# Optimization experiments

Measured on AMD Instinct MI355X. Metric: run time of the kernel, lower is better.

## Reference

```python
import jax, jax.numpy as jnp
import numpy as np

N_NODES = 10000
N_EDGES = 160000
DIM = 1024


def setup_inputs() -> dict:
    key = jax.random.key(0)
    k1, k2, k3 = jax.random.split(key, 3)
    x = jax.random.normal(k1, (N_NODES, DIM), dtype=jnp.float32)
    edge_index = jax.random.randint(k2, (2, N_EDGES), 0, N_NODES, dtype=jnp.int64)
    # Glorot-style init for the GCNConv weight; zero bias (PyG default)
    W = jax.random.normal(k3, (DIM, DIM), dtype=jnp.float32) * (1.0 / np.sqrt(DIM))
    b = jnp.zeros((DIM,), dtype=jnp.float32)
    return {"x": x, "edge_index": edge_index, "W": W, "b": b}


def reference(x, edge_index, W, b):
    """GCNConv (add_self_loops=True, symmetric norm) -> Dropout(eval=identity) -> ReLU."""
    n = x.shape[0]
    loops = jnp.arange(n, dtype=edge_index.dtype)
    src = jnp.concatenate([edge_index[0], loops])  # [E+N]
    dst = jnp.concatenate([edge_index[1], loops])  # [E+N]

    # symmetric normalization: deg^{-1/2}[src] * deg^{-1/2}[dst], deg on dst side
    deg = jax.ops.segment_sum(jnp.ones_like(dst, dtype=x.dtype), dst, num_segments=n)
    dinv = jnp.where(deg > 0, jax.lax.rsqrt(deg), jnp.zeros_like(deg))
    norm = dinv[src] * dinv[dst]  # [E+N]

    h = x @ W                                   # [N, D] dense transform first
    msg = h[src] * norm[:, None]                # gather + edge scaling [E+N, D]
    out = jax.ops.segment_sum(msg, dst, num_segments=n) + b  # scatter-add + bias

    # Dropout(0.5) is identity in eval mode; activation is ReLU
    return jax.nn.relu(out)
```

## Files before the change

kernel.cpp:

```cpp
#include <hip/hip_runtime.h>
#include <hip/hip_bf16.h>
#include <cstdint>
#include <cstddef>

typedef __bf16 bf16x8 __attribute__((ext_vector_type(8)));
typedef float  f32x4  __attribute__((ext_vector_type(4)));
typedef float  f32x2  __attribute__((ext_vector_type(2)));

#define D_DIM 1024
#define BM 128
#define BN 128
#define NXCD 8
#define CAP 64

#define GLB(p) ((const __attribute__((address_space(1))) void*)(p))
#define LDS(p) ((__attribute__((address_space(3))) void*)(p))

__global__ __launch_bounds__(256) void prep_kernel(
    const float* __restrict__ x, __bf16* __restrict__ xb,
    const float* __restrict__ W, __bf16* __restrict__ wT,
    const int* __restrict__ ei, int* __restrict__ cnt, int* __restrict__ col,
    int N, int MP, int E, int nconv, int ntr)
{
    int blk = blockIdx.x, tid = threadIdx.x;
    if (blk < nconv) {
        int i = blk * 256 + tid;
        int total = MP * (D_DIM / 8);
        if (i >= total) return;
        int row = i >> 7;
        size_t base = (size_t)i * 8;
        bf16x8 o;
        if (row < N) {
            float4 v0 = *(const float4*)(x + base);
            float4 v1 = *(const float4*)(x + base + 4);
            o[0] = (__bf16)v0.x; o[1] = (__bf16)v0.y; o[2] = (__bf16)v0.z; o[3] = (__bf16)v0.w;
            o[4] = (__bf16)v1.x; o[5] = (__bf16)v1.y; o[6] = (__bf16)v1.z; o[7] = (__bf16)v1.w;
        } else {
            #pragma unroll
            for (int j = 0; j < 8; ++j) o[j] = (__bf16)0.f;
        }
        *(bf16x8*)(xb + base) = o;
    } else if (blk < nconv + ntr) {
        __shared__ float tile[32][33];
        int bb = blk - nconv;
        int nb = (bb & 31) * 32, kb = (bb >> 5) * 32;
        int tx = tid & 31, ty = tid >> 5;
        #pragma unroll
        for (int i = 0; i < 32; i += 8)
            tile[ty + i][tx] = W[(size_t)(kb + ty + i) * D_DIM + nb + tx];
        __syncthreads();
        #pragma unroll
        for (int i = 0; i < 32; i += 8)
            wT[(size_t)(nb + ty + i) * D_DIM + kb + tx] = (__bf16)tile[tx][ty + i];
    } else {
        int e = (blk - nconv - ntr) * 256 + tid;
        if (e < E) {
            const int* src = ei;
            const int* dst = ei + E;
            int d = dst[e];
            int pos = atomicAdd(&cnt[d], 1);
            if (pos < CAP) col[(d << 6) + pos] = src[e] << 11;
        }
    }
}

__global__ __launch_bounds__(256) void gemmpad_kernel(
    const __bf16* __restrict__ A,
    const __bf16* __restrict__ BT,
    __bf16* __restrict__ C,
    const int* __restrict__ cnt, int* __restrict__ col, int Nn,
    int mtiles, int ntiles, int chunk, int npad)
{
    int tid = threadIdx.x;
    if ((int)blockIdx.x < npad) {
        int d = blockIdx.x * 256 + tid;
        if (d < Nn) {
            int c  = min(cnt[d], CAP);
            int p1 = (c + 7) & ~7;
            int zoff = Nn << 11;
            for (int p = c; p < p1; ++p) col[(d << 6) + p] = zoff;
        }
        return;
    }
    __shared__ __bf16 As[2][BM * 32];
    __shared__ __bf16 Bs[2][BN * 32];

    int wg = blockIdx.x - npad;
    int c8 = wg & (NXCD - 1);
    int r  = wg >> 3;
    int bm = c8 * chunk + r / ntiles;
    int bn = r % ntiles;
    if (bm >= mtiles) return;

    int wid = tid >> 6, lane = tid & 63;
    int wr = wid >> 1, wc = wid & 1;

    auto stage = [&](int h, int sel) {
        #pragma unroll
        for (int i = 0; i < 2; ++i) {
            int c   = i * 256 + tid;
            int row = c >> 2;
            int js  = (c & 3) ^ (row & 3);
            const __bf16* ga = A  + (size_t)(bm * BM + row) * D_DIM + h * 32 + js * 8;
            const __bf16* gb = BT + (size_t)(bn * BN + row) * D_DIM + h * 32 + js * 8;
            __builtin_amdgcn_global_load_lds(GLB(ga), LDS(&As[sel][c * 8]), 16, 0, 0);
            __builtin_amdgcn_global_load_lds(GLB(gb), LDS(&Bs[sel][c * 8]), 16, 0, 0);
        }
    };

    f32x4 acc[4][4] = {};
    stage(0, 0);
    asm volatile("s_waitcnt vmcnt(0)" ::: "memory");
    __syncthreads();

    const int halves = D_DIM / 32;
    for (int h = 0; h < halves; ++h) {
        int cur = h & 1;
        if (h + 1 < halves) stage(h + 1, cur ^ 1);
        bf16x8 af[4], bfr[4];
        int j = lane >> 4;
        #pragma unroll
        for (int mi = 0; mi < 4; ++mi) {
            int rr = wr * 64 + mi * 16 + (lane & 15);
            af[mi] = *(const bf16x8*)(&As[cur][rr * 32 + ((j ^ (rr & 3)) << 3)]);
        }
        #pragma unroll
        for (int ni = 0; ni < 4; ++ni) {
            int rr = wc * 64 + ni * 16 + (lane & 15);
            bfr[ni] = *(const bf16x8*)(&Bs[cur][rr * 32 + ((j ^ (rr & 3)) << 3)]);
        }
        #pragma unroll
        for (int mi = 0; mi < 4; ++mi)
            #pragma unroll
            for (int ni = 0; ni < 4; ++ni)
                acc[mi][ni] = __builtin_amdgcn_mfma_f32_16x16x32_bf16(
                    af[mi], bfr[ni], acc[mi][ni], 0, 0, 0);
        __syncthreads();
    }

    #pragma unroll
    for (int mi = 0; mi < 4; ++mi)
        #pragma unroll
        for (int rr = 0; rr < 4; ++rr) {
            int row = bm * BM + wr * 64 + mi * 16 + (lane >> 4) * 4 + rr;
            float dvr = 0.0f;
            if (row < Nn) dvr = rsqrtf((float)min(cnt[row], CAP) + 1.0f);
            #pragma unroll
            for (int ni = 0; ni < 4; ++ni) {
                int colc = bn * BN + wc * 64 + ni * 16 + (lane & 15);
                C[(size_t)row * D_DIM + colc] = (__bf16)(acc[mi][ni][rr] * dvr);
            }
        }
}

__global__ __launch_bounds__(256) void scatter_kernel(
    const __bf16* __restrict__ h, const int* __restrict__ cnt,
    const int* __restrict__ col, const float* __restrict__ bias,
    float* __restrict__ out, int N)
{
    int blk = blockIdx.x;
    int c   = blk & (NXCD - 1);
    int q   = blk >> 3;
    int wid = threadIdx.x >> 6, lane = threadIdx.x & 63;
    int d = q * 4 + wid;
    if (d >= N) return;

    const char* hb = (const char*)h + (size_t)c * 256;
    int lane4 = lane * 4;

    uint32_t su = *(const uint32_t*)(hb + (((uint32_t)d << 11) + lane4));
    f32x2 a;
    a[0] = __uint_as_float(su << 16);
    a[1] = __uint_as_float(su & 0xffff0000u);

    int cdeg = min(cnt[d], CAP);
    int r0 = d << 6;
    int r1 = r0 + ((cdeg + 7) & ~7);
    for (int e = r0; e < r1; e += 8) {
        int4 c0 = *(const int4*)(col + e);
        int4 c1 = *(const int4*)(col + e + 4);
        uint32_t u[8];
        u[0] = *(const uint32_t*)(hb + ((uint32_t)c0.x + lane4));
        u[1] = *(const uint32_t*)(hb + ((uint32_t)c0.y + lane4));
        u[2] = *(const uint32_t*)(hb + ((uint32_t)c0.z + lane4));
        u[3] = *(const uint32_t*)(hb + ((uint32_t)c0.w + lane4));
        u[4] = *(const uint32_t*)(hb + ((uint32_t)c1.x + lane4));
        u[5] = *(const uint32_t*)(hb + ((uint32_t)c1.y + lane4));
        u[6] = *(const uint32_t*)(hb + ((uint32_t)c1.z + lane4));
        u[7] = *(const uint32_t*)(hb + ((uint32_t)c1.w + lane4));
        #pragma unroll
        for (int t = 0; t < 8; ++t) {
            f32x2 v;
            v[0] = __uint_as_float(u[t] << 16);
            v[1] = __uint_as_float(u[t] & 0xffff0000u);
            a += v;
        }
    }

    float dv = rsqrtf((float)cdeg + 1.0f);
    int cbase = c * 128 + lane * 2;
    f32x2 bb = *(const f32x2*)(bias + cbase);
    f32x2 o;
    o[0] = fmaxf(fmaf(a[0], dv, bb[0]), 0.f);
    o[1] = fmaxf(fmaf(a[1], dv, bb[1]), 0.f);
    __builtin_nontemporal_store(o, (f32x2*)(out + (size_t)d * D_DIM + cbase));
}

extern "C" void kernel_launch(void* const* d_in, const int* in_sizes, int n_in,
                              void* d_out, int out_size, void* d_ws, size_t ws_size,
                              hipStream_t stream)
{
    const float* x  = (const float*)d_in[0];
    const int*   ei = (const int*)d_in[1];
    const float* W  = (const float*)d_in[2];
    const float* b  = (const float*)d_in[3];
    float* out = (float*)d_out;

    const int N = in_sizes[0] / D_DIM;
    const int E = in_sizes[1] / 2;
    const int MP = ((N + BM - 1) / BM) * BM;

    char* ws = (char*)d_ws;
    size_t off = 0;
    auto alloc = [&](size_t bytes) -> char* {
        char* p = ws + off;
        off += (bytes + 255) & ~(size_t)255;
        return p;
    };
    __bf16* xb  = (__bf16*)alloc((size_t)MP * D_DIM * 2);
    __bf16* wT  = (__bf16*)alloc((size_t)D_DIM * D_DIM * 2);
    __bf16* h   = (__bf16*)alloc((size_t)MP * D_DIM * 2);
    int*    cnt = (int*)alloc((size_t)N * 4);
    int*    col = (int*)alloc((size_t)N * CAP * 4);
    (void)ws_size;

    (void)hipMemsetAsync(cnt, 0, (size_t)N * 4, stream);

    int nconv = (MP * (D_DIM / 8) + 255) / 256;
    int ntr   = (D_DIM / 32) * (D_DIM / 32);
    int ncnt  = (E + 255) / 256;
    prep_kernel<<<nconv + ntr + ncnt, 256, 0, stream>>>(x, xb, W, wT, ei,
                                                        cnt, col, N, MP, E,
                                                        nconv, ntr);

    int mtiles = MP / BM;
    int ntiles = D_DIM / BN;
    int chunk  = (mtiles + NXCD - 1) / NXCD;
    int ngem   = NXCD * chunk * ntiles;
    int npad   = (N + 255) / 256;
    gemmpad_kernel<<<npad + ngem, 256, 0, stream>>>(xb, wT, h, cnt, col, N,
                                                    mtiles, ntiles, chunk, npad);

    int sblocks = ((N + 3) / 4) * NXCD;
    scatter_kernel<<<sblocks, 256, 0, stream>>>(h, cnt, col, b, out, N);
}
```

Measured before the change: 101.1 us.

## Widen scatter gathers to 8-byte loads split across half-waves; tweak GEMM LDS swizzle

```diff
diff --git a/kernel.cpp b/kernel.cpp
--- a/kernel.cpp
+++ b/kernel.cpp
@@ -100,7 +100,7 @@
         for (int i = 0; i < 2; ++i) {
             int c   = i * 256 + tid;
             int row = c >> 2;
-            int js  = (c & 3) ^ (row & 3);
+            int js  = (c & 3) ^ ((row ^ (row >> 2)) & 3);
             const __bf16* ga = A  + (size_t)(bm * BM + row) * D_DIM + h * 32 + js * 8;
             const __bf16* gb = BT + (size_t)(bn * BN + row) * D_DIM + h * 32 + js * 8;
             __builtin_amdgcn_global_load_lds(GLB(ga), LDS(&As[sel][c * 8]), 16, 0, 0);
@@ -122,12 +122,14 @@
         #pragma unroll
         for (int mi = 0; mi < 4; ++mi) {
             int rr = wr * 64 + mi * 16 + (lane & 15);
-            af[mi] = *(const bf16x8*)(&As[cur][rr * 32 + ((j ^ (rr & 3)) << 3)]);
+            int sw = (rr ^ (rr >> 2)) & 3;
+            af[mi] = *(const bf16x8*)(&As[cur][rr * 32 + ((j ^ sw) << 3)]);
         }
         #pragma unroll
         for (int ni = 0; ni < 4; ++ni) {
             int rr = wc * 64 + ni * 16 + (lane & 15);
-            bfr[ni] = *(const bf16x8*)(&Bs[cur][rr * 32 + ((j ^ (rr & 3)) << 3)]);
+            int sw = (rr ^ (rr >> 2)) & 3;
+            bfr[ni] = *(const bf16x8*)(&Bs[cur][rr * 32 + ((j ^ sw) << 3)]);
         }
         #pragma unroll
         for (int mi = 0; mi < 4; ++mi)
@@ -165,13 +167,17 @@
     int d = q * 4 + wid;
     if (d >= N) return;
 
-    const char* hb = (const char*)h + (size_t)c * 256;
-    int lane4 = lane * 4;
-
-    uint32_t su = *(const uint32_t*)(hb + (((uint32_t)d << 11) + lane4));
-    f32x2 a;
-    a[0] = __uint_as_float(su << 16);
-    a[1] = __uint_as_float(su & 0xffff0000u);
+    int half = lane >> 5;
+    int cl   = lane & 31;
+    const char* hb = (const char*)h + (size_t)c * 256 + cl * 8;
+
+    uint2 su = *(const uint2*)(hb + ((uint32_t)d << 11));
+    float gate = half ? 0.0f : 1.0f;
+    f32x2 a0, a1;
+    a0[0] = __uint_as_float(su.x << 16) * gate;
+    a0[1] = __uint_as_float(su.x & 0xffff0000u) * gate;
+    a1[0] = __uint_as_float(su.y << 16) * gate;
+    a1[1] = __uint_as_float(su.y & 0xffff0000u) * gate;
 
     int cdeg = min(cnt[d], CAP);
     int r0 = d << 6;
@@ -179,31 +185,44 @@
     for (int e = r0; e < r1; e += 8) {
         int4 c0 = *(const int4*)(col + e);
         int4 c1 = *(const int4*)(col + e + 4);
-        uint32_t u[8];
-        u[0] = *(const uint32_t*)(hb + ((uint32_t)c0.x + lane4));
-        u[1] = *(const uint32_t*)(hb + ((uint32_t)c0.y + lane4));
-        u[2] = *(const uint32_t*)(hb + ((uint32_t)c0.z + lane4));
-        u[3] = *(const uint32_t*)(hb + ((uint32_t)c0.w + lane4));
-        u[4] = *(const uint32_t*)(hb + ((uint32_t)c1.x + lane4));
-        u[5] = *(const uint32_t*)(hb + ((uint32_t)c1.y + lane4));
-        u[6] = *(const uint32_t*)(hb + ((uint32_t)c1.z + lane4));
-        u[7] = *(const uint32_t*)(hb + ((uint32_t)c1.w + lane4));
-        #pragma unroll
-        for (int t = 0; t < 8; ++t) {
-            f32x2 v;
-            v[0] = __uint_as_float(u[t] << 16);
-            v[1] = __uint_as_float(u[t] & 0xffff0000u);
-            a += v;
-        }
-    }
-
-    float dv = rsqrtf((float)cdeg + 1.0f);
-    int cbase = c * 128 + lane * 2;
-    f32x2 bb = *(const f32x2*)(bias + cbase);
-    f32x2 o;
-    o[0] = fmaxf(fmaf(a[0], dv, bb[0]), 0.f);
-    o[1] = fmaxf(fmaf(a[1], dv, bb[1]), 0.f);
-    __builtin_nontemporal_store(o, (f32x2*)(out + (size_t)d * D_DIM + cbase));
+        int o0 = half ? c0.y : c0.x;
+        int o1 = half ? c0.w : c0.z;
+        int o2 = half ? c1.y : c1.x;
+        int o3 = half ? c1.w : c1.z;
+        uint2 u0 = *(const uint2*)(hb + (uint32_t)o0);
+        uint2 u1 = *(const uint2*)(hb + (uint32_t)o1);
+        uint2 u2 = *(const uint2*)(hb + (uint32_t)o2);
+        uint2 u3 = *(const uint2*)(hb + (uint32_t)o3);
+        #pragma unroll
+        for (int t = 0; t < 4; ++t) {
+            uint2 u = t == 0 ? u0 : t == 1 ? u1 : t == 2 ? u2 : u3;
+            f32x2 v0, v1;
+            v0[0] = __uint_as_float(u.x << 16);
+            v0[1] = __uint_as_float(u.x & 0xffff0000u);
+            v1[0] = __uint_as_float(u.y << 16);
+            v1[1] = __uint_as_float(u.y & 0xffff0000u);
+            a0 += v0;
+            a1 += v1;
+        }
+    }
+
+    #pragma unroll
+    for (int j = 0; j < 2; ++j) {
+        a0[j] += __shfl_xor(a0[j], 32);
+        a1[j] += __shfl_xor(a1[j], 32);
+    }
+
+    if (half == 0) {
+        float dv = rsqrtf((float)cdeg + 1.0f);
+        int cbase = c * 128 + cl * 4;
+        float4 bb = *(const float4*)(bias + cbase);
+        f32x4 o;
+        o[0] = fmaxf(fmaf(a0[0], dv, bb.x), 0.f);
+        o[1] = fmaxf(fmaf(a0[1], dv, bb.y), 0.f);
+        o[2] = fmaxf(fmaf(a1[0], dv, bb.z), 0.f);
+        o[3] = fmaxf(fmaf(a1[1], dv, bb.w), 0.f);
+        __builtin_nontemporal_store(o, (f32x4*)(out + (size_t)d * D_DIM + cbase));
+    }
 }
 
 extern "C" void kernel_launch(void* const* d_in, const int* in_sizes, int n_in,
```

Result: slower. 110.1 us (+8.9%).
